# Performance work log

Hardware: AMD Instinct MI355X
Metric: run time of the kernel (lower is better)

Reference implementation:

```python
import jax, jax.numpy as jnp
import numpy as np

B, N, D, E, R = 4, 4096, 64, 131072, 64

def setup_inputs() -> dict:
    key = jax.random.key(0)
    k1, k2, k3, k4 = jax.random.split(key, 4)
    z = jax.random.normal(k1, (B, N, D), dtype=jnp.float32)
    pairs = jax.random.randint(k2, (E, 2), 0, N, dtype=jnp.int64)
    # Linear params (PyTorch convention: y = x @ W.T + b), init scale ~ 1/sqrt(fan_in)
    W1 = jax.random.normal(k3, (R, 4 * D), dtype=jnp.float32) / np.sqrt(4 * D)
    b1 = jnp.zeros((R,), dtype=jnp.float32)
    W2 = jax.random.normal(k4, (R, R), dtype=jnp.float32) / np.sqrt(R)
    b2 = jnp.zeros((R,), dtype=jnp.float32)
    return {"z": z, "pairs": pairs, "W1": W1, "b1": b1, "W2": W2, "b2": b2}

def reference(z, pairs, W1, b1, W2, b2):
    # gather endpoint embeddings: [B, E, D]
    zi = z[:, pairs[:, 0], :]
    zj = z[:, pairs[:, 1], :]
    # pair feature [B, E, 4D]: concat(zi, zj, zi-zj, zi*zj)
    pair = jnp.concatenate([zi, zj, zi - zj, zi * zj], axis=-1)
    # 2-layer MLP (dropout is identity at inference)
    h = jnp.einsum('bef,rf->ber', pair, W1) + b1
    h = jax.nn.relu(h)
    h = jnp.einsum('ber,sr->bes', h, W2) + b2
    return h
```

## Files before the change

### kernel.cpp

```cpp
#include <hip/hip_runtime.h>
#include <hip/hip_bf16.h>
#include <stdint.h>


typedef __attribute__((ext_vector_type(8)))  __bf16 bf16x8;
typedef __attribute__((ext_vector_type(4)))  float  f32x4;
typedef __attribute__((ext_vector_type(16))) float  f32x16;
typedef __attribute__((ext_vector_type(4)))  uint32_t u32x4;

#define E_TOT 131072
#define N_TOK 4096
#define ROWS_PER_BLOCK 512
#define NSUB 4
#define Z_ELEMS (4 * N_TOK * 64)

__global__ __launch_bounds__(256) void zcast_kernel(const float* __restrict__ z,
                                                    __bf16* __restrict__ zb)
{
    const int t = blockIdx.x * 256 + threadIdx.x;
    const float4 a = ((const float4*)z)[2 * t];
    const float4 b = ((const float4*)z)[2 * t + 1];
    bf16x8 r;
    r[0] = (__bf16)a.x; r[1] = (__bf16)a.y; r[2] = (__bf16)a.z; r[3] = (__bf16)a.w;
    r[4] = (__bf16)b.x; r[5] = (__bf16)b.y; r[6] = (__bf16)b.z; r[7] = (__bf16)b.w;
    ((bf16x8*)zb)[t] = r;
}

__device__ __forceinline__ f32x16 mfma32(bf16x8 a, bf16x8 b, f32x16 c) {
    return __builtin_amdgcn_mfma_f32_32x32x16_bf16(a, b, c, 0, 0, 0);
}

__device__ __forceinline__ bf16x8 pk8(float4 a, float4 b) {
    bf16x8 r;
    r[0] = (__bf16)a.x; r[1] = (__bf16)a.y; r[2] = (__bf16)a.z; r[3] = (__bf16)a.w;
    r[4] = (__bf16)b.x; r[5] = (__bf16)b.y; r[6] = (__bf16)b.z; r[7] = (__bf16)b.w;
    return r;
}
__device__ __forceinline__ float4 f4add(float4 a, float4 b){ return make_float4(a.x+b.x, a.y+b.y, a.z+b.z, a.w+b.w); }
__device__ __forceinline__ float4 f4sub(float4 a, float4 b){ return make_float4(a.x-b.x, a.y-b.y, a.z-b.z, a.w-b.w); }

__device__ __forceinline__ bf16x8 bmul(bf16x8 a, bf16x8 b) {
    bf16x8 r;
#pragma unroll
    for (int t = 0; t < 8; ++t)
        r[t] = (__bf16)((float)a[t] * (float)b[t]);
    return r;
}

__device__ __forceinline__ uint32_t cvtpk(float lo, float hi) {
    uint32_t w;
    asm("v_cvt_pk_bf16_f32 %0, %1, %2" : "=v"(w) : "v"(lo), "v"(hi));
    return w;
}

__device__ __forceinline__ void epi(const f32x16 acc, bf16x8& fA, bf16x8& fB) {
    float v[16];
#pragma unroll
    for (int t = 0; t < 16; ++t) v[t] = fmaxf(acc[t], 0.f);
    uint32_t w00 = cvtpk(v[0],  v[1]);
    uint32_t w01 = cvtpk(v[2],  v[3]);
    uint32_t w10 = cvtpk(v[4],  v[5]);
    uint32_t w11 = cvtpk(v[6],  v[7]);
    uint32_t w20 = cvtpk(v[8],  v[9]);
    uint32_t w21 = cvtpk(v[10], v[11]);
    uint32_t w30 = cvtpk(v[12], v[13]);
    uint32_t w31 = cvtpk(v[14], v[15]);
    asm("v_permlane32_swap_b32 %0, %1" : "+v"(w00), "+v"(w10));
    asm("v_permlane32_swap_b32 %0, %1" : "+v"(w01), "+v"(w11));
    asm("v_permlane32_swap_b32 %0, %1" : "+v"(w20), "+v"(w30));
    asm("v_permlane32_swap_b32 %0, %1" : "+v"(w21), "+v"(w31));
    u32x4 a = {w00, w01, w10, w11};
    u32x4 b = {w20, w21, w30, w31};
    fA = __builtin_bit_cast(bf16x8, a);
    fB = __builtin_bit_cast(bf16x8, b);
}

__device__ __forceinline__ f32x16 bias_init(const float* tb, int base) {
    f32x16 a;
#pragma unroll
    for (int p = 0; p < 4; ++p) {
        f32x4 c = *(const f32x4*)(tb + base + 4 * p);
        a[4*p+0] = c[0]; a[4*p+1] = c[1]; a[4*p+2] = c[2]; a[4*p+3] = c[3];
    }
    return a;
}

__global__ __launch_bounds__(256, 4) void PairRelationEncoder_62775241998442_kernel(
    const __bf16* __restrict__ zw, const int* __restrict__ pairs,
    const float* __restrict__ W1, const float* __restrict__ b1,
    const float* __restrict__ W2, const float* __restrict__ b2,
    float* __restrict__ out)
{
    const int tid  = threadIdx.x;
    const int wave = tid >> 6;
    const int lane = tid & 63;
    const int el = lane & 31;
    const int hi = lane >> 5;

    const int bid = (int)(blockIdx.x & 7) * 128 + ((int)blockIdx.x >> 3);
    const int m0 = bid * ROWS_PER_BLOCK;
    const int b  = m0 >> 17;
    const int e0 = m0 & (E_TOT - 1);
    const __bf16* zb = zw + ((size_t)b * N_TOK * 64);

    int2 ijv[NSUB];
#pragma unroll
    for (int st = 0; st < NSUB; ++st)
        ijv[st] = *(const int2*)(pairs + 2 * (size_t)(e0 + (st * 4 + wave) * 32 + el));

    __shared__ __bf16 w1s[64 * 192];
    __shared__ __bf16 w2s[64 * 64];
    __shared__ float  tb1[64];
    __shared__ float  tb2[64];

    {
        const int part = tid >> 6;
        const int scol = tid & 63;
        const int cswz = (scol & 7) << 4;
        if (part < 3) {
            const float* wr = W1 + (size_t)scol * 256;
            char* dst = (char*)w1s + scol * 384;
#pragma unroll
            for (int c8 = 0; c8 < 8; ++c8) {
                float4 p0, p1;
                if (part == 0) {
                    float4 a0 = *(const float4*)(wr + c8*8);
                    float4 a1 = *(const float4*)(wr + c8*8 + 4);
                    float4 c0 = *(const float4*)(wr + 128 + c8*8);
                    float4 c1 = *(const float4*)(wr + 128 + c8*8 + 4);
                    p0 = f4add(a0, c0); p1 = f4add(a1, c1);
                } else if (part == 1) {
                    float4 a0 = *(const float4*)(wr + 64 + c8*8);
                    float4 a1 = *(const float4*)(wr + 64 + c8*8 + 4);
                    float4 c0 = *(const float4*)(wr + 128 + c8*8);
                    float4 c1 = *(const float4*)(wr + 128 + c8*8 + 4);
                    p0 = f4sub(a0, c0); p1 = f4sub(a1, c1);
                } else {
                    p0 = *(const float4*)(wr + 192 + c8*8);
                    p1 = *(const float4*)(wr + 192 + c8*8 + 4);
                }
                *(bf16x8*)(dst + ((part * 128 + c8 * 16) ^ cswz)) = pk8(p0, p1);
            }
        } else {
            const float* wr = W2 + (size_t)scol * 64;
            char* dst = (char*)w2s + scol * 128;
#pragma unroll
            for (int c8 = 0; c8 < 8; ++c8) {
                float4 p0 = *(const float4*)(wr + c8*8);
                float4 p1 = *(const float4*)(wr + c8*8 + 4);
                *(bf16x8*)(dst + ((c8 * 16) ^ cswz)) = pk8(p0, p1);
            }
        }
        if (tid < 64)
            tb1[tid] = b1[((tid >> 4) & 1) * 32 + (tid & 3) + 8 * ((tid >> 2) & 3) + 4 * (tid >> 5)];
        else if (tid < 128) {
            const int t = tid - 64;
            tb2[t] = b2[((t >> 4) & 1) * 32 + (t & 3) + 8 * ((t >> 2) & 3) + 4 * (t >> 5)];
        }
    }

    __syncthreads();

    const int sw = (el & 7) << 4;
    const char* w1b = (const char*)w1s;
    const char* w2b = (const char*)w2s;

#pragma unroll
    for (int st = 0; st < NSUB; ++st) {
        const __bf16* zri = zb + (size_t)ijv[st].x * 64;
        const __bf16* zrj = zb + (size_t)ijv[st].y * 64;

        f32x16 acc0 = bias_init(tb1, hi * 32);
        f32x16 acc1 = bias_init(tb1, hi * 32 + 16);

#pragma unroll
        for (int q = 0; q < 4; ++q) {
            bf16x8 ziq = *(const bf16x8*)(zri + q * 16 + hi * 8);
            bf16x8 zjq = *(const bf16x8*)(zrj + q * 16 + hi * 8);
            bf16x8 pq  = bmul(ziq, zjq);
            {
                const int ko = (q * 32 + hi * 16) ^ sw;
                acc0 = mfma32(*(const bf16x8*)(w1b + (size_t)el * 384        + ko), ziq, acc0);
                acc1 = mfma32(*(const bf16x8*)(w1b + (size_t)(32 + el) * 384 + ko), ziq, acc1);
            }
            {
                const int ko = ((4 + q) * 32 + hi * 16) ^ sw;
                acc0 = mfma32(*(const bf16x8*)(w1b + (size_t)el * 384        + ko), zjq, acc0);
                acc1 = mfma32(*(const bf16x8*)(w1b + (size_t)(32 + el) * 384 + ko), zjq, acc1);
            }
            {
                const int ko = ((8 + q) * 32 + hi * 16) ^ sw;
                acc0 = mfma32(*(const bf16x8*)(w1b + (size_t)el * 384        + ko), pq, acc0);
                acc1 = mfma32(*(const bf16x8*)(w1b + (size_t)(32 + el) * 384 + ko), pq, acc1);
            }
        }

        bf16x8 F0, F1, F2, F3;
        epi(acc0, F0, F1);
        epi(acc1, F2, F3);

        f32x16 o0 = bias_init(tb2, hi * 32);
        f32x16 o1 = bias_init(tb2, hi * 32 + 16);

#pragma unroll
        for (int k2 = 0; k2 < 4; ++k2) {
            bf16x8 pf = (k2 == 0) ? F0 : (k2 == 1) ? F1 : (k2 == 2) ? F2 : F3;
            const int ko = (k2 * 32 + hi * 16) ^ sw;
            bf16x8 a0 = *(const bf16x8*)(w2b + (size_t)el * 128        + ko);
            bf16x8 a1 = *(const bf16x8*)(w2b + (size_t)(32 + el) * 128 + ko);
            o0 = mfma32(a0, pf, o0);
            o1 = mfma32(a1, pf, o1);
        }

        float* orow = out + ((size_t)(m0 + (st * 4 + wave) * 32 + el)) * 64;
#pragma unroll
        for (int p = 0; p < 4; ++p) {
            f32x4 s0v = {o0[4*p], o0[4*p+1], o0[4*p+2], o0[4*p+3]};
            f32x4 s1v = {o1[4*p], o1[4*p+1], o1[4*p+2], o1[4*p+3]};
            *(f32x4*)(orow +      8 * p + 4 * hi) = s0v;
            *(f32x4*)(orow + 32 + 8 * p + 4 * hi) = s1v;
        }
    }
}

extern "C" void kernel_launch(void* const* d_in, const int* in_sizes, int n_in,
                              void* d_out, int out_size, void* d_ws, size_t ws_size,
                              hipStream_t stream) {
    const float* z     = (const float*)d_in[0];
    const int*   pairs = (const int*)  d_in[1];
    const float* W1    = (const float*)d_in[2];
    const float* b1    = (const float*)d_in[3];
    const float* W2    = (const float*)d_in[4];
    const float* b2    = (const float*)d_in[5];
    float* out = (float*)d_out;
    __bf16* zw = (__bf16*)d_ws;

    zcast_kernel<<<Z_ELEMS / (256 * 8), 256, 0, stream>>>(z, zw);

    const int total_rows = 4 * E_TOT;
    dim3 grid(total_rows / ROWS_PER_BLOCK);
    PairRelationEncoder_62775241998442_kernel<<<grid, 256, 0, stream>>>(
        zw, pairs, W1, b1, W2, b2, out);
}
```

Baseline: 56.41 us.

## Precompute bf16 weight image once in prep kernel and halve rows per block

```diff
diff --git a/kernel.cpp b/kernel.cpp
--- a/kernel.cpp
+++ b/kernel.cpp
@@ -10,25 +10,12 @@
 
 #define E_TOT 131072
 #define N_TOK 4096
-#define ROWS_PER_BLOCK 512
-#define NSUB 4
+#define ROWS_PER_BLOCK 256
+#define NSUB 2
 #define Z_ELEMS (4 * N_TOK * 64)
-
-__global__ __launch_bounds__(256) void zcast_kernel(const float* __restrict__ z,
-                                                    __bf16* __restrict__ zb)
-{
-    const int t = blockIdx.x * 256 + threadIdx.x;
-    const float4 a = ((const float4*)z)[2 * t];
-    const float4 b = ((const float4*)z)[2 * t + 1];
-    bf16x8 r;
-    r[0] = (__bf16)a.x; r[1] = (__bf16)a.y; r[2] = (__bf16)a.z; r[3] = (__bf16)a.w;
-    r[4] = (__bf16)b.x; r[5] = (__bf16)b.y; r[6] = (__bf16)b.z; r[7] = (__bf16)b.w;
-    ((bf16x8*)zb)[t] = r;
-}
-
-__device__ __forceinline__ f32x16 mfma32(bf16x8 a, bf16x8 b, f32x16 c) {
-    return __builtin_amdgcn_mfma_f32_32x32x16_bf16(a, b, c, 0, 0, 0);
-}
+#define WIMG_OFF (Z_ELEMS * 2)
+#define WIMG_B1 32768
+#define WIMG_B2 33024
 
 __device__ __forceinline__ bf16x8 pk8(float4 a, float4 b) {
     bf16x8 r;
@@ -38,6 +25,65 @@
 }
 __device__ __forceinline__ float4 f4add(float4 a, float4 b){ return make_float4(a.x+b.x, a.y+b.y, a.z+b.z, a.w+b.w); }
 __device__ __forceinline__ float4 f4sub(float4 a, float4 b){ return make_float4(a.x-b.x, a.y-b.y, a.z-b.z, a.w-b.w); }
+
+__global__ __launch_bounds__(256) void prep_kernel(
+    const float* __restrict__ z, const float* __restrict__ W1, const float* __restrict__ b1,
+    const float* __restrict__ W2, const float* __restrict__ b2,
+    __bf16* __restrict__ zw, char* __restrict__ wimg)
+{
+    const int tid = threadIdx.x;
+    const int blk = blockIdx.x;
+    if (blk < 512) {
+        const int t = blk * 256 + tid;
+        const float4 a = ((const float4*)z)[2 * t];
+        const float4 b = ((const float4*)z)[2 * t + 1];
+        ((bf16x8*)zw)[t] = pk8(a, b);
+        return;
+    }
+    const int part = tid >> 6;
+    const int scol = tid & 63;
+    const int cswz = (scol & 7) << 4;
+    if (part < 3) {
+        const float* wr = W1 + (size_t)scol * 256;
+        char* dst = wimg + scol * 384;
+#pragma unroll
+        for (int c8 = 0; c8 < 8; ++c8) {
+            float4 p0, p1;
+            if (part == 0) {
+                float4 a0 = *(const float4*)(wr + c8*8);
+                float4 a1 = *(const float4*)(wr + c8*8 + 4);
+                float4 c0 = *(const float4*)(wr + 128 + c8*8);
+                float4 c1 = *(const float4*)(wr + 128 + c8*8 + 4);
+                p0 = f4add(a0, c0); p1 = f4add(a1, c1);
+            } else if (part == 1) {
+                float4 a0 = *(const float4*)(wr + 64 + c8*8);
+                float4 a1 = *(const float4*)(wr + 64 + c8*8 + 4);
+                float4 c0 = *(const float4*)(wr + 128 + c8*8);
+                float4 c1 = *(const float4*)(wr + 128 + c8*8 + 4);
+                p0 = f4sub(a0, c0); p1 = f4sub(a1, c1);
+            } else {
+                p0 = *(const float4*)(wr + 192 + c8*8);
+                p1 = *(const float4*)(wr + 192 + c8*8 + 4);
+            }
+            *(bf16x8*)(dst + ((part * 128 + c8 * 16) ^ cswz)) = pk8(p0, p1);
+        }
+    } else {
+        const float* wr = W2 + (size_t)scol * 64;
+        char* dst = wimg + 24576 + scol * 128;
+#pragma unroll
+        for (int c8 = 0; c8 < 8; ++c8) {
+            float4 p0 = *(const float4*)(wr + c8*8);
+            float4 p1 = *(const float4*)(wr + c8*8 + 4);
+            *(bf16x8*)(dst + ((c8 * 16) ^ cswz)) = pk8(p0, p1);
+        }
+    }
+    if (tid < 64)            *(float*)(wimg + WIMG_B1 + 4 * tid) = b1[tid];
+    else if (tid < 128)      *(float*)(wimg + WIMG_B2 + 4 * (tid - 64)) = b2[tid - 64];
+}
+
+__device__ __forceinline__ f32x16 mfma32(bf16x8 a, bf16x8 b, f32x16 c) {
+    return __builtin_amdgcn_mfma_f32_32x32x16_bf16(a, b, c, 0, 0, 0);
+}
 
 __device__ __forceinline__ bf16x8 bmul(bf16x8 a, bf16x8 b) {
     bf16x8 r;
@@ -86,10 +132,8 @@
 }
 
 __global__ __launch_bounds__(256, 4) void PairRelationEncoder_62775241998442_kernel(
-    const __bf16* __restrict__ zw, const int* __restrict__ pairs,
-    const float* __restrict__ W1, const float* __restrict__ b1,
-    const float* __restrict__ W2, const float* __restrict__ b2,
-    float* __restrict__ out)
+    const __bf16* __restrict__ zw, const char* __restrict__ wimg,
+    const int* __restrict__ pairs, float* __restrict__ out)
 {
     const int tid  = threadIdx.x;
     const int wave = tid >> 6;
@@ -97,7 +141,7 @@
     const int el = lane & 31;
     const int hi = lane >> 5;
 
-    const int bid = (int)(blockIdx.x & 7) * 128 + ((int)blockIdx.x >> 3);
+    const int bid = (int)(blockIdx.x & 7) * 256 + ((int)blockIdx.x >> 3);
     const int m0 = bid * ROWS_PER_BLOCK;
     const int b  = m0 >> 17;
     const int e0 = m0 & (E_TOT - 1);
@@ -108,62 +152,30 @@
     for (int st = 0; st < NSUB; ++st)
         ijv[st] = *(const int2*)(pairs + 2 * (size_t)(e0 + (st * 4 + wave) * 32 + el));
 
-    __shared__ __bf16 w1s[64 * 192];
-    __shared__ __bf16 w2s[64 * 64];
-    __shared__ float  tb1[64];
-    __shared__ float  tb2[64];
-
-    {
-        const int part = tid >> 6;
-        const int scol = tid & 63;
-        const int cswz = (scol & 7) << 4;
-        if (part < 3) {
-            const float* wr = W1 + (size_t)scol * 256;
-            char* dst = (char*)w1s + scol * 384;
-#pragma unroll
-            for (int c8 = 0; c8 < 8; ++c8) {
-                float4 p0, p1;
-                if (part == 0) {
-                    float4 a0 = *(const float4*)(wr + c8*8);
-                    float4 a1 = *(const float4*)(wr + c8*8 + 4);
-                    float4 c0 = *(const float4*)(wr + 128 + c8*8);
-                    float4 c1 = *(const float4*)(wr + 128 + c8*8 + 4);
-                    p0 = f4add(a0, c0); p1 = f4add(a1, c1);
-                } else if (part == 1) {
-                    float4 a0 = *(const float4*)(wr + 64 + c8*8);
-                    float4 a1 = *(const float4*)(wr + 64 + c8*8 + 4);
-                    float4 c0 = *(const float4*)(wr + 128 + c8*8);
-                    float4 c1 = *(const float4*)(wr + 128 + c8*8 + 4);
-                    p0 = f4sub(a0, c0); p1 = f4sub(a1, c1);
-                } else {
-                    p0 = *(const float4*)(wr + 192 + c8*8);
-                    p1 = *(const float4*)(wr + 192 + c8*8 + 4);
-                }
-                *(bf16x8*)(dst + ((part * 128 + c8 * 16) ^ cswz)) = pk8(p0, p1);
-            }
-        } else {
-            const float* wr = W2 + (size_t)scol * 64;
-            char* dst = (char*)w2s + scol * 128;
-#pragma unroll
-            for (int c8 = 0; c8 < 8; ++c8) {
-                float4 p0 = *(const float4*)(wr + c8*8);
-                float4 p1 = *(const float4*)(wr + c8*8 + 4);
-                *(bf16x8*)(dst + ((c8 * 16) ^ cswz)) = pk8(p0, p1);
-            }
-        }
-        if (tid < 64)
-            tb1[tid] = b1[((tid >> 4) & 1) * 32 + (tid & 3) + 8 * ((tid >> 2) & 3) + 4 * (tid >> 5)];
-        else if (tid < 128) {
-            const int t = tid - 64;
-            tb2[t] = b2[((t >> 4) & 1) * 32 + (t & 3) + 8 * ((t >> 2) & 3) + 4 * (t >> 5)];
-        }
+    __shared__ char lds[33280];
+    const char* w1b = lds;
+    const char* w2b = lds + 24576;
+    float* tb1 = (float*)(lds + 32768);
+    float* tb2 = (float*)(lds + 33024);
+
+#pragma unroll
+    for (int r = 0; r < 8; ++r) {
+        const int off = (r * 256 + tid) * 16;
+        float4 v = *(const float4*)(wimg + off);
+        *(float4*)(lds + off) = v;
+    }
+    if (tid < 64)
+        tb1[tid] = *(const float*)(wimg + WIMG_B1 +
+                   4 * (((tid >> 4) & 1) * 32 + (tid & 3) + 8 * ((tid >> 2) & 3) + 4 * (tid >> 5)));
+    else if (tid < 128) {
+        const int t = tid - 64;
+        tb2[t] = *(const float*)(wimg + WIMG_B2 +
+                 4 * (((t >> 4) & 1) * 32 + (t & 3) + 8 * ((t >> 2) & 3) + 4 * (t >> 5)));
     }
 
     __syncthreads();
 
     const int sw = (el & 7) << 4;
-    const char* w1b = (const char*)w1s;
-    const char* w2b = (const char*)w2s;
 
 #pragma unroll
     for (int st = 0; st < NSUB; ++st) {
@@ -233,12 +245,13 @@
     const float* W2    = (const float*)d_in[4];
     const float* b2    = (const float*)d_in[5];
     float* out = (float*)d_out;
-    __bf16* zw = (__bf16*)d_ws;
-
-    zcast_kernel<<<Z_ELEMS / (256 * 8), 256, 0, stream>>>(z, zw);
+    __bf16* zw  = (__bf16*)d_ws;
+    char*   img = (char*)d_ws + WIMG_OFF;
+
+    prep_kernel<<<513, 256, 0, stream>>>(z, W1, b1, W2, b2, zw, img);
 
     const int total_rows = 4 * E_TOT;
     dim3 grid(total_rows / ROWS_PER_BLOCK);
     PairRelationEncoder_62775241998442_kernel<<<grid, 256, 0, stream>>>(
-        zw, pairs, W1, b1, W2, b2, out);
-}
+        zw, img, pairs, out);
+}
```

New measurement: 50.34 us. -10.8%, faster.
